# Kernel optimization log

Measured on AMD Instinct MI355X. Metric: run time of the kernel, lower is better.

Reference implementation:

```python
import jax, jax.numpy as jnp
import numpy as np

N_NODES = 100000


def gcn_conv(x, edge_src, edge_dst, edge_weight, W, b):
    # support = x @ W ; out = A @ support + b  (A given as weighted edge list)
    h = x @ W                                   # [N, d_out]
    msg = h[edge_src] * edge_weight[:, None]     # [E, d_out]
    agg = jax.ops.segment_sum(msg, edge_dst, num_segments=N_NODES)
    return agg + b


def setup_inputs() -> dict:
    key = jax.random.key(0)
    ks = jax.random.split(key, 8)
    N, E, m, hidden, m_y = N_NODES, 1600000, 128, 64, 32
    x = jax.random.normal(ks[0], (N, m), dtype=jnp.float32)
    edge_src = jax.random.randint(ks[1], (E,), 0, N, dtype=jnp.int32)
    edge_dst = jax.random.randint(ks[2], (E,), 0, N, dtype=jnp.int32)
    edge_weight = jax.random.uniform(ks[3], (E,), dtype=jnp.float32)
    s1 = 1.0 / np.sqrt(m)
    s2 = 1.0 / np.sqrt(hidden)
    W1 = jax.random.uniform(ks[4], (m, hidden), dtype=jnp.float32, minval=-s1, maxval=s1)
    b1 = jax.random.uniform(ks[5], (hidden,), dtype=jnp.float32, minval=-s1, maxval=s1)
    W2 = jax.random.uniform(ks[6], (hidden, m_y), dtype=jnp.float32, minval=-s2, maxval=s2)
    b2 = jax.random.uniform(ks[7], (m_y,), dtype=jnp.float32, minval=-s2, maxval=s2)
    return {"x": x, "edge_src": edge_src, "edge_dst": edge_dst,
            "edge_weight": edge_weight, "W1": W1, "b1": b1, "W2": W2, "b2": b2}


def reference(x, edge_src, edge_dst, edge_weight, W1, b1, W2, b2):
    out = gcn_conv(x, edge_src, edge_dst, edge_weight, W1, b1)
    out = jax.nn.relu(out)
    # F.dropout(p=0.5, training=self.training) -> identity in eval mode
    out = gcn_conv(out, edge_src, edge_dst, edge_weight, W2, b2)
    return out
```

## Files before the change

kernel.cpp:

```cpp
#include <hip/hip_runtime.h>
#include <hip/hip_bf16.h>


typedef unsigned short u16;
typedef unsigned int uint;
typedef short short8 __attribute__((ext_vector_type(8)));
typedef float floatx4 __attribute__((ext_vector_type(4)));

static __device__ __forceinline__ u16 f2bf(float f) {
    unsigned int u = __float_as_uint(f);
    return (u16)((u + 0x7fff + ((u >> 16) & 1)) >> 16);
}

#define F4C(v, j) ((j)==0?(v).x:((j)==1?(v).y:((j)==2?(v).z:(v).w)))
#define CHUNK 2048
#define ECAP 384

__global__ __launch_bounds__(256) void init_kernel(
    const float* __restrict__ W1, u16* __restrict__ wfg, int* __restrict__ gcursor)
{
    const int idx = blockIdx.x * 256 + threadIdx.x;
    if (idx < 512) gcursor[idx] = 0;
    const float4 v = ((const float4*)W1)[idx];
    const int k = idx >> 4, n4 = (idx & 15) * 4;
    const int step = k >> 5, klane = (k >> 3) & 3, j = k & 7;
    #pragma unroll
    for (int c = 0; c < 4; c++) {
        int n = n4 + c;
        wfg[(((n >> 4) * 4 + step) * 64 + klane * 16 + (n & 15)) * 8 + j] = f2bf(F4C(v, c));
    }
}

union __align__(16) SharedU {
    struct {
        u16 xs[64][136];
        u16 wf[4][4][64][8];
    } g;
    struct {
        int2 stage[CHUNK];
        u16  stb[CHUNK];
        int  hist[512], sc[512], xscan[512], place[512], runbase[512];
    } p;
};

__global__ __launch_bounds__(256, 4) void g1p_kernel(
    const float* __restrict__ x, const u16* __restrict__ wfg,
    u16* __restrict__ h1, int N,
    const int* __restrict__ src, const int* __restrict__ dst,
    const float* __restrict__ w, int* __restrict__ gcursor,
    int2* __restrict__ es, int E, int cap, int pblocks)
{
    __shared__ SharedU sh;
    const int tid = threadIdx.x;

    if (blockIdx.x < pblocks) {
        const int base = blockIdx.x * CHUNK;
        const int nloc = min(CHUNK, E - base);

        sh.p.hist[tid] = 0; sh.p.hist[tid + 256] = 0;
        __syncthreads();
        for (int i = tid; i < nloc; i += 256)
            atomicAdd(&sh.p.hist[dst[base + i] >> 8], 1);
        __syncthreads();

        sh.p.sc[tid] = sh.p.hist[tid];
        sh.p.sc[tid + 256] = sh.p.hist[tid + 256];
        __syncthreads();
        for (int o = 1; o < 512; o <<= 1) {
            int v0 = (tid >= o) ? sh.p.sc[tid - o] : 0;
            int v1 = (tid + 256 >= o) ? sh.p.sc[tid + 256 - o] : 0;
            __syncthreads();
            sh.p.sc[tid] += v0;
            sh.p.sc[tid + 256] += v1;
            __syncthreads();
        }
        sh.p.xscan[tid] = sh.p.sc[tid] - sh.p.hist[tid];
        sh.p.xscan[tid + 256] = sh.p.sc[tid + 256] - sh.p.hist[tid + 256];
        sh.p.place[tid] = sh.p.xscan[tid];
        sh.p.place[tid + 256] = sh.p.xscan[tid + 256];
        __syncthreads();

        for (int i = tid; i < nloc; i += 256) {
            int d = dst[base + i];
            int b = d >> 8;
            int pos = atomicAdd(&sh.p.place[b], 1);
            sh.p.stage[pos] = make_int2(src[base + i] | ((d & 255) << 24),
                                        __float_as_int(w[base + i]));
            sh.p.stb[pos] = (u16)b;
        }
        __syncthreads();

        {
            int l0 = sh.p.hist[tid], l1 = sh.p.hist[tid + 256];
            sh.p.runbase[tid]       = l0 ? atomicAdd(&gcursor[tid], l0)       : 0;
            sh.p.runbase[tid + 256] = l1 ? atomicAdd(&gcursor[tid + 256], l1) : 0;
        }
        __syncthreads();

        for (int i = tid; i < nloc; i += 256) {
            int b = sh.p.stb[i];
            es[(size_t)b * cap + sh.p.runbase[b] + (i - sh.p.xscan[b])] = sh.p.stage[i];
        }
        return;
    }

    const int row0 = (blockIdx.x - pblocks) * 64;
    {
        const float4* wg4 = (const float4*)wfg;
        float4* wl4 = (float4*)&sh.g.wf[0][0][0][0];
        #pragma unroll
        for (int i = 0; i < 4; i++) wl4[tid + i*256] = wg4[tid + i*256];
    }
    {
        const float4* x4 = (const float4*)x;
        #pragma unroll
        for (int i = 0; i < 8; i++) {
            int idx = tid + i*256;
            int r = idx >> 5, kc = idx & 31;
            int gr = row0 + r;
            float4 v = make_float4(0.f,0.f,0.f,0.f);
            if (gr < N) v = x4[gr*32 + kc];
            ushort4 o;
            o.x = f2bf(v.x); o.y = f2bf(v.y); o.z = f2bf(v.z); o.w = f2bf(v.w);
            *(ushort4*)&sh.g.xs[r][kc*4] = o;
        }
    }
    __syncthreads();

    const int wave = tid >> 6, lane = tid & 63;
    const int m = lane & 15, quad = lane >> 4;
    const int rw = wave * 16;

    floatx4 acc[4] = {(floatx4)(0.f), (floatx4)(0.f), (floatx4)(0.f), (floatx4)(0.f)};
    #pragma unroll
    for (int step = 0; step < 4; step++) {
        short8 a = *(const short8*)&sh.g.xs[rw + m][step*32 + quad*8];
        #pragma unroll
        for (int nt = 0; nt < 4; nt++) {
            short8 b = *(const short8*)&sh.g.wf[nt][step][lane][0];
            acc[nt] = __builtin_amdgcn_mfma_f32_16x16x32_bf16(a, b, acc[nt], 0, 0, 0);
        }
    }
    #pragma unroll
    for (int nt = 0; nt < 4; nt++) {
        #pragma unroll
        for (int r = 0; r < 4; r++) {
            int gr = row0 + rw + quad*4 + r;
            if (gr < N) h1[(size_t)gr*64 + nt*16 + m] = f2bf(acc[nt][r]);
        }
    }
}

#define SCAP 6144
__global__ __launch_bounds__(512, 3) void sort2_kernel(
    const int2* __restrict__ es, const int* __restrict__ gcursor,
    int2* __restrict__ es2, int2* __restrict__ off2, int N, int cap, int nb)
{
    __shared__ int2 stage[SCAP];
    __shared__ int hist[256], sc[256], cur[256];
    const int t = threadIdx.x;
    const int b = blockIdx.x;
    const int e0 = b * cap;
    const int len = gcursor[b];
    const int nstage = min(len, SCAP);

    if (t < 256) hist[t] = 0;
    __syncthreads();
    for (int i = t; i < nstage; i += 512) {
        int2 e = es[e0 + i];
        stage[i] = e;
        atomicAdd(&hist[((unsigned)e.x) >> 24], 1);
    }
    for (int i = SCAP + t; i < len; i += 512)
        atomicAdd(&hist[((unsigned)es[e0 + i].x) >> 24], 1);
    __syncthreads();

    int v = 0;
    if (t < 256) { v = hist[t]; sc[t] = v; }
    __syncthreads();
    for (int o = 1; o < 256; o <<= 1) {
        int add = 0;
        if (t < 256 && t >= o) add = sc[t - o];
        __syncthreads();
        if (t < 256) sc[t] += add;
        __syncthreads();
    }
    if (t < 256) {
        int ex = sc[t] - v;
        cur[t] = ex;
        int g = b * 256 + t;
        if (g < N) off2[g] = make_int2(e0 + ex, e0 + ex + v);
    }
    __syncthreads();

    for (int i = t; i < nstage; i += 512) {
        int2 e = stage[i];
        int pos = e0 + atomicAdd(&cur[((unsigned)e.x) >> 24], 1);
        es2[pos] = e;
    }
    for (int i = SCAP + t; i < len; i += 512) {
        int2 e = es[e0 + i];
        int pos = e0 + atomicAdd(&cur[((unsigned)e.x) >> 24], 1);
        es2[pos] = e;
    }
}

__global__ __launch_bounds__(256, 4) void gather1_kernel(
    const u16* __restrict__ h1, const int2* __restrict__ es,
    const int2* __restrict__ off2, const float* __restrict__ b1,
    const float* __restrict__ W2, u16* __restrict__ h2, int N)
{
    __shared__ __align__(16) u16 ts[64][72];
    __shared__ __align__(16) u16 wf2[2][2][64][8];
    __shared__ float b1s[64];
    __shared__ int2 eb[4][ECAP];
    const int tid = threadIdx.x;

    {
        const float4* s4 = (const float4*)W2;
        #pragma unroll
        for (int i = 0; i < 2; i++) {
            int idx = tid + i*256;
            float4 v = s4[idx];
            int k = idx >> 3, n4 = (idx & 7) * 4;
            int step = k >> 5, quad = (k >> 3) & 3, j = k & 7;
            #pragma unroll
            for (int c = 0; c < 4; c++) {
                int n = n4 + c;
                wf2[n >> 4][step][quad*16 + (n & 15)][j] = f2bf(F4C(v, c));
            }
        }
        if (tid < 16) ((float4*)b1s)[tid] = ((const float4*)b1)[tid];
    }
    __syncthreads();

    const int wave = tid >> 6, lane = tid & 63;
    const int h = lane >> 4, fl = lane & 15;
    const int node0 = blockIdx.x * 64 + wave * 16;
    const uint2* h1v = (const uint2*)h1;
    uint* tsu = (uint*)&ts[0][0];

    const int2 sg = off2[min(node0 + fl, N - 1)];
    const int beg = __builtin_amdgcn_readfirstlane(sg.x);
    const int end = __builtin_amdgcn_readlane(sg.y, 15);
    const int len = end - beg;

    if (len <= ECAP) {
        for (int k = lane; k < len; k += 64) eb[wave][k] = es[beg + k];

        #pragma unroll 1
        for (int j = 0; j < 8; j++) {
            const int pbegA = __builtin_amdgcn_readlane(sg.x, j) - beg;
            const int pendA = __builtin_amdgcn_readlane(sg.y, j) - beg;
            const int pbegB = __builtin_amdgcn_readlane(sg.x, j + 8) - beg;
            const int pendB = __builtin_amdgcn_readlane(sg.y, j + 8) - beg;
            const int clA = max(pendA - 1, 0), clB = max(pendB - 1, 0);
            float a0 = 0.f, a1 = 0.f, a2 = 0.f, a3 = 0.f;
            float c0 = 0.f, c1 = 0.f, c2 = 0.f, c3 = 0.f;
            int pA = pbegA, pB = pbegB;
            #pragma unroll 1
            while (pA < pendA || pB < pendB) {
                const int iA0 = pA + h,     iA1 = pA + 4 + h;
                const int iA2 = pA + 8 + h, iA3 = pA + 12 + h;
                const int iB0 = pB + h,     iB1 = pB + 4 + h;
                const int iB2 = pB + 8 + h, iB3 = pB + 12 + h;
                int2 eA0 = eb[wave][min(iA0, clA)];
                int2 eA1 = eb[wave][min(iA1, clA)];
                int2 eA2 = eb[wave][min(iA2, clA)];
                int2 eA3 = eb[wave][min(iA3, clA)];
                int2 eB0 = eb[wave][min(iB0, clB)];
                int2 eB1 = eb[wave][min(iB1, clB)];
                int2 eB2 = eb[wave][min(iB2, clB)];
                int2 eB3 = eb[wave][min(iB3, clB)];
                uint2 vA0 = h1v[(size_t)(eA0.x & 0xFFFFFF) * 16 + fl];
                uint2 vA1 = h1v[(size_t)(eA1.x & 0xFFFFFF) * 16 + fl];
                uint2 vA2 = h1v[(size_t)(eA2.x & 0xFFFFFF) * 16 + fl];
                uint2 vA3 = h1v[(size_t)(eA3.x & 0xFFFFFF) * 16 + fl];
                uint2 vB0 = h1v[(size_t)(eB0.x & 0xFFFFFF) * 16 + fl];
                uint2 vB1 = h1v[(size_t)(eB1.x & 0xFFFFFF) * 16 + fl];
                uint2 vB2 = h1v[(size_t)(eB2.x & 0xFFFFFF) * 16 + fl];
                uint2 vB3 = h1v[(size_t)(eB3.x & 0xFFFFFF) * 16 + fl];
                float wA0 = (iA0 < pendA) ? __int_as_float(eA0.y) : 0.f;
                float wA1 = (iA1 < pendA) ? __int_as_float(eA1.y) : 0.f;
                float wA2 = (iA2 < pendA) ? __int_as_float(eA2.y) : 0.f;
                float wA3 = (iA3 < pendA) ? __int_as_float(eA3.y) : 0.f;
                float wB0 = (iB0 < pendB) ? __int_as_float(eB0.y) : 0.f;
                float wB1 = (iB1 < pendB) ? __int_as_float(eB1.y) : 0.f;
                float wB2 = (iB2 < pendB) ? __int_as_float(eB2.y) : 0.f;
                float wB3 = (iB3 < pendB) ? __int_as_float(eB3.y) : 0.f;
                a0 += __uint_as_float(vA0.x << 16) * wA0 + __uint_as_float(vA1.x << 16) * wA1
                    + __uint_as_float(vA2.x << 16) * wA2 + __uint_as_float(vA3.x << 16) * wA3;
                a1 += __uint_as_float(vA0.x & 0xFFFF0000u) * wA0 + __uint_as_float(vA1.x & 0xFFFF0000u) * wA1
                    + __uint_as_float(vA2.x & 0xFFFF0000u) * wA2 + __uint_as_float(vA3.x & 0xFFFF0000u) * wA3;
                a2 += __uint_as_float(vA0.y << 16) * wA0 + __uint_as_float(vA1.y << 16) * wA1
                    + __uint_as_float(vA2.y << 16) * wA2 + __uint_as_float(vA3.y << 16) * wA3;
                a3 += __uint_as_float(vA0.y & 0xFFFF0000u) * wA0 + __uint_as_float(vA1.y & 0xFFFF0000u) * wA1
                    + __uint_as_float(vA2.y & 0xFFFF0000u) * wA2 + __uint_as_float(vA3.y & 0xFFFF0000u) * wA3;
                c0 += __uint_as_float(vB0.x << 16) * wB0 + __uint_as_float(vB1.x << 16) * wB1
                    + __uint_as_float(vB2.x << 16) * wB2 + __uint_as_float(vB3.x << 16) * wB3;
                c1 += __uint_as_float(vB0.x & 0xFFFF0000u) * wB0 + __uint_as_float(vB1.x & 0xFFFF0000u) * wB1
                    + __uint_as_float(vB2.x & 0xFFFF0000u) * wB2 + __uint_as_float(vB3.x & 0xFFFF0000u) * wB3;
                c2 += __uint_as_float(vB0.y << 16) * wB0 + __uint_as_float(vB1.y << 16) * wB1
                    + __uint_as_float(vB2.y << 16) * wB2 + __uint_as_float(vB3.y << 16) * wB3;
                c3 += __uint_as_float(vB0.y & 0xFFFF0000u) * wB0 + __uint_as_float(vB1.y & 0xFFFF0000u) * wB1
                    + __uint_as_float(vB2.y & 0xFFFF0000u) * wB2 + __uint_as_float(vB3.y & 0xFFFF0000u) * wB3;
                pA += 16; pB += 16;
            }
            a0 += __shfl_xor(a0, 16, 64); a1 += __shfl_xor(a1, 16, 64);
            a2 += __shfl_xor(a2, 16, 64); a3 += __shfl_xor(a3, 16, 64);
            a0 += __shfl_xor(a0, 32, 64); a1 += __shfl_xor(a1, 32, 64);
            a2 += __shfl_xor(a2, 32, 64); a3 += __shfl_xor(a3, 32, 64);
            c0 += __shfl_xor(c0, 16, 64); c1 += __shfl_xor(c1, 16, 64);
            c2 += __shfl_xor(c2, 16, 64); c3 += __shfl_xor(c3, 16, 64);
            c0 += __shfl_xor(c0, 32, 64); c1 += __shfl_xor(c1, 32, 64);
            c2 += __shfl_xor(c2, 32, 64); c3 += __shfl_xor(c3, 32, 64);
            if (h == 0) {
                uint t0 = (uint)f2bf(fmaxf(a0 + b1s[4*fl],     0.f))
                        | ((uint)f2bf(fmaxf(a1 + b1s[4*fl + 1], 0.f)) << 16);
                uint t1 = (uint)f2bf(fmaxf(a2 + b1s[4*fl + 2], 0.f))
                        | ((uint)f2bf(fmaxf(a3 + b1s[4*fl + 3], 0.f)) << 16);
                *(uint2*)&tsu[(wave*16 + j) * 36 + 2*fl] = make_uint2(t0, t1);
                uint t2 = (uint)f2bf(fmaxf(c0 + b1s[4*fl],     0.f))
                        | ((uint)f2bf(fmaxf(c1 + b1s[4*fl + 1], 0.f)) << 16);
                uint t3 = (uint)f2bf(fmaxf(c2 + b1s[4*fl + 2], 0.f))
                        | ((uint)f2bf(fmaxf(c3 + b1s[4*fl + 3], 0.f)) << 16);
                *(uint2*)&tsu[(wave*16 + j + 8) * 36 + 2*fl] = make_uint2(t2, t3);
            }
        }
    } else {
        #pragma unroll 1
        for (int i = 0; i < 16; i++) {
            const int pbeg = __builtin_amdgcn_readlane(sg.x, i);
            const int pend = __builtin_amdgcn_readlane(sg.y, i);
            const int cl = max(pend - 1, 0);
            float a0 = 0.f, a1 = 0.f, a2 = 0.f, a3 = 0.f;
            #pragma unroll 1
            for (int p = pbeg; p < pend; p += 16) {
                const int i0 = p + h, i1 = p + 4 + h, i2 = p + 8 + h, i3 = p + 12 + h;
                int2 e0 = es[min(i0, cl)];
                int2 e1 = es[min(i1, cl)];
                int2 e2 = es[min(i2, cl)];
                int2 e3 = es[min(i3, cl)];
                uint2 v0 = h1v[(size_t)(e0.x & 0xFFFFFF) * 16 + fl];
                uint2 v1 = h1v[(size_t)(e1.x & 0xFFFFFF) * 16 + fl];
                uint2 v2 = h1v[(size_t)(e2.x & 0xFFFFFF) * 16 + fl];
                uint2 v3 = h1v[(size_t)(e3.x & 0xFFFFFF) * 16 + fl];
                float w0 = (i0 < pend) ? __int_as_float(e0.y) : 0.f;
                float w1 = (i1 < pend) ? __int_as_float(e1.y) : 0.f;
                float w2 = (i2 < pend) ? __int_as_float(e2.y) : 0.f;
                float w3 = (i3 < pend) ? __int_as_float(e3.y) : 0.f;
                a0 += __uint_as_float(v0.x << 16) * w0 + __uint_as_float(v1.x << 16) * w1
                    + __uint_as_float(v2.x << 16) * w2 + __uint_as_float(v3.x << 16) * w3;
                a1 += __uint_as_float(v0.x & 0xFFFF0000u) * w0 + __uint_as_float(v1.x & 0xFFFF0000u) * w1
                    + __uint_as_float(v2.x & 0xFFFF0000u) * w2 + __uint_as_float(v3.x & 0xFFFF0000u) * w3;
                a2 += __uint_as_float(v0.y << 16) * w0 + __uint_as_float(v1.y << 16) * w1
                    + __uint_as_float(v2.y << 16) * w2 + __uint_as_float(v3.y << 16) * w3;
                a3 += __uint_as_float(v0.y & 0xFFFF0000u) * w0 + __uint_as_float(v1.y & 0xFFFF0000u) * w1
                    + __uint_as_float(v2.y & 0xFFFF0000u) * w2 + __uint_as_float(v3.y & 0xFFFF0000u) * w3;
            }
            a0 += __shfl_xor(a0, 16, 64); a1 += __shfl_xor(a1, 16, 64);
            a2 += __shfl_xor(a2, 16, 64); a3 += __shfl_xor(a3, 16, 64);
            a0 += __shfl_xor(a0, 32, 64); a1 += __shfl_xor(a1, 32, 64);
            a2 += __shfl_xor(a2, 32, 64); a3 += __shfl_xor(a3, 32, 64);
            if (h == 0) {
                uint t0 = (uint)f2bf(fmaxf(a0 + b1s[4*fl],     0.f))
                        | ((uint)f2bf(fmaxf(a1 + b1s[4*fl + 1], 0.f)) << 16);
                uint t1 = (uint)f2bf(fmaxf(a2 + b1s[4*fl + 2], 0.f))
                        | ((uint)f2bf(fmaxf(a3 + b1s[4*fl + 3], 0.f)) << 16);
                *(uint2*)&tsu[(wave*16 + i) * 36 + 2*fl] = make_uint2(t0, t1);
            }
        }
    }

    const int m = lane & 15, quad = lane >> 4;
    floatx4 acc[2] = {(floatx4)(0.f), (floatx4)(0.f)};
    #pragma unroll
    for (int step = 0; step < 2; step++) {
        short8 a = *(const short8*)&ts[wave*16 + m][step*32 + quad*8];
        #pragma unroll
        for (int nt = 0; nt < 2; nt++) {
            short8 b = *(const short8*)&wf2[nt][step][lane][0];
            acc[nt] = __builtin_amdgcn_mfma_f32_16x16x32_bf16(a, b, acc[nt], 0, 0, 0);
        }
    }
    #pragma unroll
    for (int nt = 0; nt < 2; nt++) {
        #pragma unroll
        for (int r = 0; r < 4; r++) {
            int g = node0 + quad*4 + r;
            if (g < N) h2[(size_t)g*32 + nt*16 + m] = f2bf(acc[nt][r]);
        }
    }
}

__global__ __launch_bounds__(256, 4) void gather2_kernel(
    const u16* __restrict__ h2, const int2* __restrict__ es,
    const int2* __restrict__ off2, const float* __restrict__ b2,
    float* __restrict__ out, int N)
{
    __shared__ int2 eb[4][ECAP];
    const int tid = threadIdx.x;
    const int wave = tid >> 6, lane = tid & 63;
    const int g = lane >> 3, fl = lane & 7;
    const int node0 = blockIdx.x * 64 + wave * 16;
    const uint2* h2v = (const uint2*)h2;

    const int2 sg = off2[min(node0 + (lane & 15), N - 1)];
    const int beg = __builtin_amdgcn_readfirstlane(sg.x);
    const int end = __builtin_amdgcn_readlane(sg.y, 15);
    const int len = end - beg;
    const float4 bb = ((const float4*)b2)[fl];

    if (len <= ECAP) {
        for (int k = lane; k < len; k += 64) eb[wave][k] = es[beg + k];

        #pragma unroll 1
        for (int j = 0; j < 8; j++) {
            const int pbegA = __builtin_amdgcn_readlane(sg.x, j) - beg;
            const int pendA = __builtin_amdgcn_readlane(sg.y, j) - beg;
            const int pbegB = __builtin_amdgcn_readlane(sg.x, j + 8) - beg;
            const int pendB = __builtin_amdgcn_readlane(sg.y, j + 8) - beg;
            const int clA = max(pendA - 1, 0), clB = max(pendB - 1, 0);
            float a0 = 0.f, a1 = 0.f, a2 = 0.f, a3 = 0.f;
            float c0 = 0.f, c1 = 0.f, c2 = 0.f, c3 = 0.f;
            int pA = pbegA, pB = pbegB;
            #pragma unroll 1
            while (pA < pendA || pB < pendB) {
                const int iA0 = pA + g, iA1 = pA + 8 + g;
                const int iB0 = pB + g, iB1 = pB + 8 + g;
                int2 eA0 = eb[wave][min(iA0, clA)];
                int2 eA1 = eb[wave][min(iA1, clA)];
                int2 eB0 = eb[wave][min(iB0, clB)];
                int2 eB1 = eb[wave][min(iB1, clB)];
                uint2 vA0 = h2v[(size_t)(eA0.x & 0xFFFFFF) * 8 + fl];
                uint2 vA1 = h2v[(size_t)(eA1.x & 0xFFFFFF) * 8 + fl];
                uint2 vB0 = h2v[(size_t)(eB0.x & 0xFFFFFF) * 8 + fl];
                uint2 vB1 = h2v[(size_t)(eB1.x & 0xFFFFFF) * 8 + fl];
                float wA0 = (iA0 < pendA) ? __int_as_float(eA0.y) : 0.f;
                float wA1 = (iA1 < pendA) ? __int_as_float(eA1.y) : 0.f;
                float wB0 = (iB0 < pendB) ? __int_as_float(eB0.y) : 0.f;
                float wB1 = (iB1 < pendB) ? __int_as_float(eB1.y) : 0.f;
                a0 += __uint_as_float(vA0.x << 16) * wA0 + __uint_as_float(vA1.x << 16) * wA1;
                a1 += __uint_as_float(vA0.x & 0xFFFF0000u) * wA0 + __uint_as_float(vA1.x & 0xFFFF0000u) * wA1;
                a2 += __uint_as_float(vA0.y << 16) * wA0 + __uint_as_float(vA1.y << 16) * wA1;
                a3 += __uint_as_float(vA0.y & 0xFFFF0000u) * wA0 + __uint_as_float(vA1.y & 0xFFFF0000u) * wA1;
                c0 += __uint_as_float(vB0.x << 16) * wB0 + __uint_as_float(vB1.x << 16) * wB1;
                c1 += __uint_as_float(vB0.x & 0xFFFF0000u) * wB0 + __uint_as_float(vB1.x & 0xFFFF0000u) * wB1;
                c2 += __uint_as_float(vB0.y << 16) * wB0 + __uint_as_float(vB1.y << 16) * wB1;
                c3 += __uint_as_float(vB0.y & 0xFFFF0000u) * wB0 + __uint_as_float(vB1.y & 0xFFFF0000u) * wB1;
                pA += 16; pB += 16;
            }
            a0 += __shfl_xor(a0, 8, 64);  a1 += __shfl_xor(a1, 8, 64);
            a2 += __shfl_xor(a2, 8, 64);  a3 += __shfl_xor(a3, 8, 64);
            a0 += __shfl_xor(a0, 16, 64); a1 += __shfl_xor(a1, 16, 64);
            a2 += __shfl_xor(a2, 16, 64); a3 += __shfl_xor(a3, 16, 64);
            a0 += __shfl_xor(a0, 32, 64); a1 += __shfl_xor(a1, 32, 64);
            a2 += __shfl_xor(a2, 32, 64); a3 += __shfl_xor(a3, 32, 64);
            c0 += __shfl_xor(c0, 8, 64);  c1 += __shfl_xor(c1, 8, 64);
            c2 += __shfl_xor(c2, 8, 64);  c3 += __shfl_xor(c3, 8, 64);
            c0 += __shfl_xor(c0, 16, 64); c1 += __shfl_xor(c1, 16, 64);
            c2 += __shfl_xor(c2, 16, 64); c3 += __shfl_xor(c3, 16, 64);
            c0 += __shfl_xor(c0, 32, 64); c1 += __shfl_xor(c1, 32, 64);
            c2 += __shfl_xor(c2, 32, 64); c3 += __shfl_xor(c3, 32, 64);
            const int dA = node0 + j, dB = node0 + j + 8;
            if (g == 0 && dA < N)
                *(float4*)&out[(size_t)dA * 32 + 4 * fl] =
                    make_float4(a0 + bb.x, a1 + bb.y, a2 + bb.z, a3 + bb.w);
            if (g == 0 && dB < N)
                *(float4*)&out[(size_t)dB * 32 + 4 * fl] =
                    make_float4(c0 + bb.x, c1 + bb.y, c2 + bb.z, c3 + bb.w);
        }
    } else {
        #pragma unroll 1
        for (int i = 0; i < 16; i++) {
            const int pbeg = __builtin_amdgcn_readlane(sg.x, i);
            const int pend = __builtin_amdgcn_readlane(sg.y, i);
            const int cl = max(pend - 1, 0);
            float a0 = 0.f, a1 = 0.f, a2 = 0.f, a3 = 0.f;
            #pragma unroll 1
            for (int p = pbeg; p < pend; p += 32) {
                const int i0 = p + g, i1 = p + 8 + g, i2 = p + 16 + g, i3 = p + 24 + g;
                int2 e0 = es[min(i0, cl)];
                int2 e1 = es[min(i1, cl)];
                int2 e2 = es[min(i2, cl)];
                int2 e3 = es[min(i3, cl)];
                uint2 v0 = h2v[(size_t)(e0.x & 0xFFFFFF) * 8 + fl];
                uint2 v1 = h2v[(size_t)(e1.x & 0xFFFFFF) * 8 + fl];
                uint2 v2 = h2v[(size_t)(e2.x & 0xFFFFFF) * 8 + fl];
                uint2 v3 = h2v[(size_t)(e3.x & 0xFFFFFF) * 8 + fl];
                float w0 = (i0 < pend) ? __int_as_float(e0.y) : 0.f;
                float w1 = (i1 < pend) ? __int_as_float(e1.y) : 0.f;
                float w2 = (i2 < pend) ? __int_as_float(e2.y) : 0.f;
                float w3 = (i3 < pend) ? __int_as_float(e3.y) : 0.f;
                a0 += __uint_as_float(v0.x << 16) * w0 + __uint_as_float(v1.x << 16) * w1
                    + __uint_as_float(v2.x << 16) * w2 + __uint_as_float(v3.x << 16) * w3;
                a1 += __uint_as_float(v0.x & 0xFFFF0000u) * w0 + __uint_as_float(v1.x & 0xFFFF0000u) * w1
                    + __uint_as_float(v2.x & 0xFFFF0000u) * w2 + __uint_as_float(v3.x & 0xFFFF0000u) * w3;
                a2 += __uint_as_float(v0.y << 16) * w0 + __uint_as_float(v1.y << 16) * w1
                    + __uint_as_float(v2.y << 16) * w2 + __uint_as_float(v3.y << 16) * w3;
                a3 += __uint_as_float(v0.y & 0xFFFF0000u) * w0 + __uint_as_float(v1.y & 0xFFFF0000u) * w1
                    + __uint_as_float(v2.y & 0xFFFF0000u) * w2 + __uint_as_float(v3.y & 0xFFFF0000u) * w3;
            }
            a0 += __shfl_xor(a0, 8, 64);  a1 += __shfl_xor(a1, 8, 64);
            a2 += __shfl_xor(a2, 8, 64);  a3 += __shfl_xor(a3, 8, 64);
            a0 += __shfl_xor(a0, 16, 64); a1 += __shfl_xor(a1, 16, 64);
            a2 += __shfl_xor(a2, 16, 64); a3 += __shfl_xor(a3, 16, 64);
            a0 += __shfl_xor(a0, 32, 64); a1 += __shfl_xor(a1, 32, 64);
            a2 += __shfl_xor(a2, 32, 64); a3 += __shfl_xor(a3, 32, 64);
            const int d = node0 + i;
            if (g == 0 && d < N)
                *(float4*)&out[(size_t)d * 32 + 4 * fl] =
                    make_float4(a0 + bb.x, a1 + bb.y, a2 + bb.z, a3 + bb.w);
        }
    }
}

extern "C" void kernel_launch(void* const* d_in, const int* in_sizes, int n_in,
                              void* d_out, int out_size, void* d_ws, size_t ws_size,
                              hipStream_t stream)
{
    const float* x   = (const float*)d_in[0];
    const int*  esrc = (const int*)d_in[1];
    const int*  edst = (const int*)d_in[2];
    const float* ew  = (const float*)d_in[3];
    const float* W1  = (const float*)d_in[4];
    const float* b1  = (const float*)d_in[5];
    const float* W2  = (const float*)d_in[6];
    const float* b2  = (const float*)d_in[7];
    float* out = (float*)d_out;

    const int N = in_sizes[0] / 128;
    const int E = in_sizes[1];
    const int nb = (N + 255) >> 8;

    const int mean = (E + nb - 1) / nb;
    int s = 1; while (s * s < mean) s++;
    const int cap = (mean + 8 * s + 15) & ~15;

    char* base = (char*)d_ws;
    size_t o = 0;
    auto alloc = [&](size_t bytes) { char* p = base + o; o = (o + bytes + 255) & ~(size_t)255; return p; };
    u16*  h1      = (u16*) alloc((size_t)N * 64 * 2);
    u16*  h2      = (u16*) alloc((size_t)N * 32 * 2);
    int2* es      = (int2*)alloc((size_t)nb * cap * 8);
    int2* es2     = (int2*)alloc((size_t)nb * cap * 8);
    int2* off2    = (int2*)alloc((size_t)N * 8);
    int*  gcursor = (int*) alloc(512 * 4);
    u16*  wfg     = (u16*) alloc(8192 * 2);

    const int pblocks = (E + CHUNK - 1) / CHUNK;
    const int gblocks = (N + 63) / 64;

    init_kernel<<<8, 256, 0, stream>>>(W1, wfg, gcursor);
    g1p_kernel<<<pblocks + gblocks, 256, 0, stream>>>(
        x, wfg, h1, N, esrc, edst, ew, gcursor, es, E, cap, pblocks);
    sort2_kernel<<<nb, 512, 0, stream>>>(es, gcursor, es2, off2, N, cap, nb);
    gather1_kernel<<<(N + 63) / 64, 256, 0, stream>>>(h1, es2, off2, b1, W2, h2, N);
    gather2_kernel<<<(N + 63) / 64, 256, 0, stream>>>(h2, es2, off2, b2, out, N);
}
```

Baseline: 221.1 us.

## Scatter edges directly to buckets and load GEMM A-operand straight to registers

```diff
diff --git a/kernel.cpp b/kernel.cpp
--- a/kernel.cpp
+++ b/kernel.cpp
@@ -33,17 +33,14 @@
 
 union __align__(16) SharedU {
     struct {
-        u16 xs[64][136];
         u16 wf[4][4][64][8];
     } g;
     struct {
-        int2 stage[CHUNK];
-        u16  stb[CHUNK];
-        int  hist[512], sc[512], xscan[512], place[512], runbase[512];
+        int hist[512], runbase[512], place[512];
     } p;
 };
 
-__global__ __launch_bounds__(256, 4) void g1p_kernel(
+__global__ __launch_bounds__(256, 5) void g1p_kernel(
     const float* __restrict__ x, const u16* __restrict__ wfg,
     u16* __restrict__ h1, int N,
     const int* __restrict__ src, const int* __restrict__ dst,
@@ -63,43 +60,21 @@
             atomicAdd(&sh.p.hist[dst[base + i] >> 8], 1);
         __syncthreads();
 
-        sh.p.sc[tid] = sh.p.hist[tid];
-        sh.p.sc[tid + 256] = sh.p.hist[tid + 256];
-        __syncthreads();
-        for (int o = 1; o < 512; o <<= 1) {
-            int v0 = (tid >= o) ? sh.p.sc[tid - o] : 0;
-            int v1 = (tid + 256 >= o) ? sh.p.sc[tid + 256 - o] : 0;
-            __syncthreads();
-            sh.p.sc[tid] += v0;
-            sh.p.sc[tid + 256] += v1;
-            __syncthreads();
-        }
-        sh.p.xscan[tid] = sh.p.sc[tid] - sh.p.hist[tid];
-        sh.p.xscan[tid + 256] = sh.p.sc[tid + 256] - sh.p.hist[tid + 256];
-        sh.p.place[tid] = sh.p.xscan[tid];
-        sh.p.place[tid + 256] = sh.p.xscan[tid + 256];
-        __syncthreads();
-
-        for (int i = tid; i < nloc; i += 256) {
-            int d = dst[base + i];
-            int b = d >> 8;
-            int pos = atomicAdd(&sh.p.place[b], 1);
-            sh.p.stage[pos] = make_int2(src[base + i] | ((d & 255) << 24),
-                                        __float_as_int(w[base + i]));
-            sh.p.stb[pos] = (u16)b;
-        }
-        __syncthreads();
-
         {
             int l0 = sh.p.hist[tid], l1 = sh.p.hist[tid + 256];
             sh.p.runbase[tid]       = l0 ? atomicAdd(&gcursor[tid], l0)       : 0;
             sh.p.runbase[tid + 256] = l1 ? atomicAdd(&gcursor[tid + 256], l1) : 0;
+            sh.p.place[tid] = 0; sh.p.place[tid + 256] = 0;
         }
         __syncthreads();
 
         for (int i = tid; i < nloc; i += 256) {
-            int b = sh.p.stb[i];
-            es[(size_t)b * cap + sh.p.runbase[b] + (i - sh.p.xscan[b])] = sh.p.stage[i];
+            int d = dst[base + i];
+            int b = d >> 8;
+            int r = atomicAdd(&sh.p.place[b], 1);
+            es[(size_t)b * cap + sh.p.runbase[b] + r] =
+                make_int2(src[base + i] | ((d & 255) << 24),
+                          __float_as_int(w[base + i]));
         }
         return;
     }
@@ -111,33 +86,32 @@
         #pragma unroll
         for (int i = 0; i < 4; i++) wl4[tid + i*256] = wg4[tid + i*256];
     }
-    {
-        const float4* x4 = (const float4*)x;
-        #pragma unroll
-        for (int i = 0; i < 8; i++) {
-            int idx = tid + i*256;
-            int r = idx >> 5, kc = idx & 31;
-            int gr = row0 + r;
-            float4 v = make_float4(0.f,0.f,0.f,0.f);
-            if (gr < N) v = x4[gr*32 + kc];
-            ushort4 o;
-            o.x = f2bf(v.x); o.y = f2bf(v.y); o.z = f2bf(v.z); o.w = f2bf(v.w);
-            *(ushort4*)&sh.g.xs[r][kc*4] = o;
-        }
-    }
-    __syncthreads();
 
     const int wave = tid >> 6, lane = tid & 63;
     const int m = lane & 15, quad = lane >> 4;
-    const int rw = wave * 16;
+    const int gr0 = row0 + wave * 16 + m;
+    const int grc = min(gr0, N - 1);
+    const float4* xr = (const float4*)x + (size_t)grc * 32;
+
+    float4 xv[8];
+    #pragma unroll
+    for (int s = 0; s < 4; s++) {
+        xv[2*s]     = xr[s*8 + quad*2];
+        xv[2*s + 1] = xr[s*8 + quad*2 + 1];
+    }
+    __syncthreads();
 
     floatx4 acc[4] = {(floatx4)(0.f), (floatx4)(0.f), (floatx4)(0.f), (floatx4)(0.f)};
     #pragma unroll
-    for (int step = 0; step < 4; step++) {
-        short8 a = *(const short8*)&sh.g.xs[rw + m][step*32 + quad*8];
+    for (int s = 0; s < 4; s++) {
+        short8 a;
+        a[0] = (short)f2bf(xv[2*s].x);   a[1] = (short)f2bf(xv[2*s].y);
+        a[2] = (short)f2bf(xv[2*s].z);   a[3] = (short)f2bf(xv[2*s].w);
+        a[4] = (short)f2bf(xv[2*s+1].x); a[5] = (short)f2bf(xv[2*s+1].y);
+        a[6] = (short)f2bf(xv[2*s+1].z); a[7] = (short)f2bf(xv[2*s+1].w);
         #pragma unroll
         for (int nt = 0; nt < 4; nt++) {
-            short8 b = *(const short8*)&sh.g.wf[nt][step][lane][0];
+            short8 b = *(const short8*)&sh.g.wf[nt][s][lane][0];
             acc[nt] = __builtin_amdgcn_mfma_f32_16x16x32_bf16(a, b, acc[nt], 0, 0, 0);
         }
     }
@@ -145,7 +119,7 @@
     for (int nt = 0; nt < 4; nt++) {
         #pragma unroll
         for (int r = 0; r < 4; r++) {
-            int gr = row0 + rw + quad*4 + r;
+            int gr = row0 + wave*16 + quad*4 + r;
             if (gr < N) h1[(size_t)gr*64 + nt*16 + m] = f2bf(acc[nt][r]);
         }
     }
```

Result: slower. 234.9 us (+6.2%).

## Split each sort2 bucket across two blocks with per-half histograms

Applied to the files above, without the earlier changes.

```diff
diff --git a/kernel.cpp b/kernel.cpp
--- a/kernel.cpp
+++ b/kernel.cpp
@@ -151,32 +151,31 @@
     }
 }
 
-#define SCAP 6144
-__global__ __launch_bounds__(512, 3) void sort2_kernel(
+#define SCAP2 2304
+__global__ __launch_bounds__(512, 4) void sort2_kernel(
     const int2* __restrict__ es, const int* __restrict__ gcursor,
     int2* __restrict__ es2, int2* __restrict__ off2, int N, int cap, int nb)
 {
-    __shared__ int2 stage[SCAP];
-    __shared__ int hist[256], sc[256], cur[256];
+    __shared__ int2 stage[SCAP2];
+    __shared__ int hA[256], hB[256], sc[256], cur[256];
     const int t = threadIdx.x;
-    const int b = blockIdx.x;
+    const int b = blockIdx.x >> 1, h = blockIdx.x & 1;
     const int e0 = b * cap;
     const int len = gcursor[b];
-    const int nstage = min(len, SCAP);
-
-    if (t < 256) hist[t] = 0;
+    const int len1 = (len + 1) >> 1;
+
+    if (t < 256) { hA[t] = 0; hB[t] = 0; }
     __syncthreads();
-    for (int i = t; i < nstage; i += 512) {
+    for (int i = t; i < len; i += 512) {
         int2 e = es[e0 + i];
-        stage[i] = e;
-        atomicAdd(&hist[((unsigned)e.x) >> 24], 1);
-    }
-    for (int i = SCAP + t; i < len; i += 512)
-        atomicAdd(&hist[((unsigned)es[e0 + i].x) >> 24], 1);
+        int k = ((unsigned)e.x) >> 24;
+        if (i < len1) { atomicAdd(&hA[k], 1); if (h == 0) stage[i] = e; }
+        else          { atomicAdd(&hB[k], 1); if (h == 1) stage[i - len1] = e; }
+    }
     __syncthreads();
 
     int v = 0;
-    if (t < 256) { v = hist[t]; sc[t] = v; }
+    if (t < 256) { v = hA[t] + hB[t]; sc[t] = v; }
     __syncthreads();
     for (int o = 1; o < 256; o <<= 1) {
         int add = 0;
@@ -187,19 +186,17 @@
     }
     if (t < 256) {
         int ex = sc[t] - v;
-        cur[t] = ex;
-        int g = b * 256 + t;
-        if (g < N) off2[g] = make_int2(e0 + ex, e0 + ex + v);
+        cur[t] = ex + (h ? hA[t] : 0);
+        if (h == 0) {
+            int g = b * 256 + t;
+            if (g < N) off2[g] = make_int2(e0 + ex, e0 + ex + v);
+        }
     }
     __syncthreads();
 
-    for (int i = t; i < nstage; i += 512) {
+    const int myn = h ? (len - len1) : len1;
+    for (int i = t; i < myn; i += 512) {
         int2 e = stage[i];
-        int pos = e0 + atomicAdd(&cur[((unsigned)e.x) >> 24], 1);
-        es2[pos] = e;
-    }
-    for (int i = SCAP + t; i < len; i += 512) {
-        int2 e = es[e0 + i];
         int pos = e0 + atomicAdd(&cur[((unsigned)e.x) >> 24], 1);
         es2[pos] = e;
     }
@@ -554,7 +551,7 @@
     init_kernel<<<8, 256, 0, stream>>>(W1, wfg, gcursor);
     g1p_kernel<<<pblocks + gblocks, 256, 0, stream>>>(
         x, wfg, h1, N, esrc, edst, ew, gcursor, es, E, cap, pblocks);
-    sort2_kernel<<<nb, 512, 0, stream>>>(es, gcursor, es2, off2, N, cap, nb);
+    sort2_kernel<<<2 * nb, 512, 0, stream>>>(es, gcursor, es2, off2, N, cap, nb);
     gather1_kernel<<<(N + 63) / 64, 256, 0, stream>>>(h1, es2, off2, b1, W2, h2, N);
     gather2_kernel<<<(N + 63) / 64, 256, 0, stream>>>(h2, es2, off2, b2, out, N);
 }
```

After: 221.5 us. No clear change (+0.1%).

## Fuse bucket sort with layer-1 gather using LDS-resident sorted edges

Applied to the files above, without the earlier changes.

```diff
diff --git a/kernel.cpp b/kernel.cpp
--- a/kernel.cpp
+++ b/kernel.cpp
@@ -14,6 +14,7 @@
 
 #define F4C(v, j) ((j)==0?(v).x:((j)==1?(v).y:((j)==2?(v).z:(v).w)))
 #define CHUNK 2048
+#define CAPC 4608
 #define ECAP 384
 
 __global__ __launch_bounds__(256) void init_kernel(
@@ -151,109 +152,89 @@
     }
 }
 
-#define SCAP 6144
-__global__ __launch_bounds__(512, 3) void sort2_kernel(
-    const int2* __restrict__ es, const int* __restrict__ gcursor,
-    int2* __restrict__ es2, int2* __restrict__ off2, int N, int cap, int nb)
+__global__ __launch_bounds__(512, 4) void sg1_kernel(
+    const u16* __restrict__ h1, const int2* __restrict__ es,
+    const int* __restrict__ gcursor, int2* __restrict__ es2,
+    int2* __restrict__ off2, const float* __restrict__ b1,
+    const float* __restrict__ W2, u16* __restrict__ h2, int N, int cap)
 {
-    __shared__ int2 stage[SCAP];
-    __shared__ int hist[256], sc[256], cur[256];
+    __shared__ int2 sorted[CAPC];
+    __shared__ __align__(16) u16 ts[8][16][72];
+    __shared__ __align__(16) u16 wf2[2][2][64][8];
+    __shared__ float b1s[64];
+    __shared__ int hist[256], exs[256], cur[256];
     const int t = threadIdx.x;
     const int b = blockIdx.x;
     const int e0 = b * cap;
-    const int len = gcursor[b];
-    const int nstage = min(len, SCAP);
-
-    if (t < 256) hist[t] = 0;
-    __syncthreads();
-    for (int i = t; i < nstage; i += 512) {
-        int2 e = es[e0 + i];
-        stage[i] = e;
-        atomicAdd(&hist[((unsigned)e.x) >> 24], 1);
-    }
-    for (int i = SCAP + t; i < len; i += 512)
-        atomicAdd(&hist[((unsigned)es[e0 + i].x) >> 24], 1);
+    const int len = min(gcursor[b], CAPC);
+
+    {
+        const float4* s4 = (const float4*)W2;
+        float4 v = s4[t];
+        int k = t >> 3, n4 = (t & 7) * 4;
+        int step = k >> 5, quad = (k >> 3) & 3, j = k & 7;
+        #pragma unroll
+        for (int c = 0; c < 4; c++) {
+            int n = n4 + c;
+            wf2[n >> 4][step][quad*16 + (n & 15)][j] = f2bf(F4C(v, c));
+        }
+        if (t < 16) ((float4*)b1s)[t] = ((const float4*)b1)[t];
+        if (t < 256) hist[t] = 0;
+    }
+    __syncthreads();
+
+    int2 re[9]; int rk[9];
+    #pragma unroll
+    for (int k = 0; k < 9; k++) {
+        int i = t + k * 512;
+        if (i < len) {
+            re[k] = es[e0 + i];
+            rk[k] = (int)(((unsigned)re[k].x) >> 24);
+            atomicAdd(&hist[rk[k]], 1);
+        } else rk[k] = -1;
+    }
     __syncthreads();
 
     int v = 0;
-    if (t < 256) { v = hist[t]; sc[t] = v; }
+    if (t < 256) { v = hist[t]; cur[t] = v; }
     __syncthreads();
     for (int o = 1; o < 256; o <<= 1) {
         int add = 0;
-        if (t < 256 && t >= o) add = sc[t - o];
-        __syncthreads();
-        if (t < 256) sc[t] += add;
+        if (t < 256 && t >= o) add = cur[t - o];
+        __syncthreads();
+        if (t < 256) cur[t] += add;
         __syncthreads();
     }
     if (t < 256) {
-        int ex = sc[t] - v;
+        int ex = cur[t] - v;
+        exs[t] = ex;
         cur[t] = ex;
         int g = b * 256 + t;
         if (g < N) off2[g] = make_int2(e0 + ex, e0 + ex + v);
     }
     __syncthreads();
 
-    for (int i = t; i < nstage; i += 512) {
-        int2 e = stage[i];
-        int pos = e0 + atomicAdd(&cur[((unsigned)e.x) >> 24], 1);
-        es2[pos] = e;
-    }
-    for (int i = SCAP + t; i < len; i += 512) {
-        int2 e = es[e0 + i];
-        int pos = e0 + atomicAdd(&cur[((unsigned)e.x) >> 24], 1);
-        es2[pos] = e;
-    }
-}
-
-__global__ __launch_bounds__(256, 4) void gather1_kernel(
-    const u16* __restrict__ h1, const int2* __restrict__ es,
-    const int2* __restrict__ off2, const float* __restrict__ b1,
-    const float* __restrict__ W2, u16* __restrict__ h2, int N)
-{
-    __shared__ __align__(16) u16 ts[64][72];
-    __shared__ __align__(16) u16 wf2[2][2][64][8];
-    __shared__ float b1s[64];
-    __shared__ int2 eb[4][ECAP];
-    const int tid = threadIdx.x;
-
-    {
-        const float4* s4 = (const float4*)W2;
-        #pragma unroll
-        for (int i = 0; i < 2; i++) {
-            int idx = tid + i*256;
-            float4 v = s4[idx];
-            int k = idx >> 3, n4 = (idx & 7) * 4;
-            int step = k >> 5, quad = (k >> 3) & 3, j = k & 7;
-            #pragma unroll
-            for (int c = 0; c < 4; c++) {
-                int n = n4 + c;
-                wf2[n >> 4][step][quad*16 + (n & 15)][j] = f2bf(F4C(v, c));
-            }
-        }
-        if (tid < 16) ((float4*)b1s)[tid] = ((const float4*)b1)[tid];
-    }
-    __syncthreads();
-
-    const int wave = tid >> 6, lane = tid & 63;
+    #pragma unroll
+    for (int k = 0; k < 9; k++)
+        if (rk[k] >= 0) sorted[atomicAdd(&cur[rk[k]], 1)] = re[k];
+    __syncthreads();
+
+    for (int i = t; i < len; i += 512)
+        es2[e0 + i] = sorted[i];
+
+    const int wave = t >> 6, lane = t & 63;
     const int h = lane >> 4, fl = lane & 15;
-    const int node0 = blockIdx.x * 64 + wave * 16;
     const uint2* h1v = (const uint2*)h1;
-    uint* tsu = (uint*)&ts[0][0];
-
-    const int2 sg = off2[min(node0 + fl, N - 1)];
-    const int beg = __builtin_amdgcn_readfirstlane(sg.x);
-    const int end = __builtin_amdgcn_readlane(sg.y, 15);
-    const int len = end - beg;
-
-    if (len <= ECAP) {
-        for (int k = lane; k < len; k += 64) eb[wave][k] = es[beg + k];
-
+    uint* tsu = (uint*)&ts[wave][0][0];
+
+    #pragma unroll 1
+    for (int half = 0; half < 2; half++) {
+        const int n0 = wave * 32 + half * 16;
         #pragma unroll 1
         for (int j = 0; j < 8; j++) {
-            const int pbegA = __builtin_amdgcn_readlane(sg.x, j) - beg;
-            const int pendA = __builtin_amdgcn_readlane(sg.y, j) - beg;
-            const int pbegB = __builtin_amdgcn_readlane(sg.x, j + 8) - beg;
-            const int pendB = __builtin_amdgcn_readlane(sg.y, j + 8) - beg;
+            const int nA = n0 + j, nB = n0 + j + 8;
+            const int pbegA = exs[nA], pendA = pbegA + hist[nA];
+            const int pbegB = exs[nB], pendB = pbegB + hist[nB];
             const int clA = max(pendA - 1, 0), clB = max(pendB - 1, 0);
             float a0 = 0.f, a1 = 0.f, a2 = 0.f, a3 = 0.f;
             float c0 = 0.f, c1 = 0.f, c2 = 0.f, c3 = 0.f;
@@ -264,14 +245,14 @@
                 const int iA2 = pA + 8 + h, iA3 = pA + 12 + h;
                 const int iB0 = pB + h,     iB1 = pB + 4 + h;
                 const int iB2 = pB + 8 + h, iB3 = pB + 12 + h;
-                int2 eA0 = eb[wave][min(iA0, clA)];
-                int2 eA1 = eb[wave][min(iA1, clA)];
-                int2 eA2 = eb[wave][min(iA2, clA)];
-                int2 eA3 = eb[wave][min(iA3, clA)];
-                int2 eB0 = eb[wave][min(iB0, clB)];
-                int2 eB1 = eb[wave][min(iB1, clB)];
-                int2 eB2 = eb[wave][min(iB2, clB)];
-                int2 eB3 = eb[wave][min(iB3, clB)];
+                int2 eA0 = sorted[min(iA0, clA)];
+                int2 eA1 = sorted[min(iA1, clA)];
+                int2 eA2 = sorted[min(iA2, clA)];
+                int2 eA3 = sorted[min(iA3, clA)];
+                int2 eB0 = sorted[min(iB0, clB)];
+                int2 eB1 = sorted[min(iB1, clB)];
+                int2 eB2 = sorted[min(iB2, clB)];
+                int2 eB3 = sorted[min(iB3, clB)];
                 uint2 vA0 = h1v[(size_t)(eA0.x & 0xFFFFFF) * 16 + fl];
                 uint2 vA1 = h1v[(size_t)(eA1.x & 0xFFFFFF) * 16 + fl];
                 uint2 vA2 = h1v[(size_t)(eA2.x & 0xFFFFFF) * 16 + fl];
@@ -319,76 +300,33 @@
                         | ((uint)f2bf(fmaxf(a1 + b1s[4*fl + 1], 0.f)) << 16);
                 uint t1 = (uint)f2bf(fmaxf(a2 + b1s[4*fl + 2], 0.f))
                         | ((uint)f2bf(fmaxf(a3 + b1s[4*fl + 3], 0.f)) << 16);
-                *(uint2*)&tsu[(wave*16 + j) * 36 + 2*fl] = make_uint2(t0, t1);
+                *(uint2*)&tsu[j * 36 + 2*fl] = make_uint2(t0, t1);
                 uint t2 = (uint)f2bf(fmaxf(c0 + b1s[4*fl],     0.f))
                         | ((uint)f2bf(fmaxf(c1 + b1s[4*fl + 1], 0.f)) << 16);
                 uint t3 = (uint)f2bf(fmaxf(c2 + b1s[4*fl + 2], 0.f))
                         | ((uint)f2bf(fmaxf(c3 + b1s[4*fl + 3], 0.f)) << 16);
-                *(uint2*)&tsu[(wave*16 + j + 8) * 36 + 2*fl] = make_uint2(t2, t3);
-            }
-        }
-    } else {
-        #pragma unroll 1
-        for (int i = 0; i < 16; i++) {
-            const int pbeg = __builtin_amdgcn_readlane(sg.x, i);
-            const int pend = __builtin_amdgcn_readlane(sg.y, i);
-            const int cl = max(pend - 1, 0);
-            float a0 = 0.f, a1 = 0.f, a2 = 0.f, a3 = 0.f;
-            #pragma unroll 1
-            for (int p = pbeg; p < pend; p += 16) {
-                const int i0 = p + h, i1 = p + 4 + h, i2 = p + 8 + h, i3 = p + 12 + h;
-                int2 e0 = es[min(i0, cl)];
-                int2 e1 = es[min(i1, cl)];
-                int2 e2 = es[min(i2, cl)];
-                int2 e3 = es[min(i3, cl)];
-                uint2 v0 = h1v[(size_t)(e0.x & 0xFFFFFF) * 16 + fl];
-                uint2 v1 = h1v[(size_t)(e1.x & 0xFFFFFF) * 16 + fl];
-                uint2 v2 = h1v[(size_t)(e2.x & 0xFFFFFF) * 16 + fl];
-                uint2 v3 = h1v[(size_t)(e3.x & 0xFFFFFF) * 16 + fl];
-                float w0 = (i0 < pend) ? __int_as_float(e0.y) : 0.f;
-                float w1 = (i1 < pend) ? __int_as_float(e1.y) : 0.f;
-                float w2 = (i2 < pend) ? __int_as_float(e2.y) : 0.f;
-                float w3 = (i3 < pend) ? __int_as_float(e3.y) : 0.f;
-                a0 += __uint_as_float(v0.x << 16) * w0 + __uint_as_float(v1.x << 16) * w1
-                    + __uint_as_float(v2.x << 16) * w2 + __uint_as_float(v3.x << 16) * w3;
-                a1 += __uint_as_float(v0.x & 0xFFFF0000u) * w0 + __uint_as_float(v1.x & 0xFFFF0000u) * w1
-                    + __uint_as_float(v2.x & 0xFFFF0000u) * w2 + __uint_as_float(v3.x & 0xFFFF0000u) * w3;
-                a2 += __uint_as_float(v0.y << 16) * w0 + __uint_as_float(v1.y << 16) * w1
-                    + __uint_as_float(v2.y << 16) * w2 + __uint_as_float(v3.y << 16) * w3;
-                a3 += __uint_as_float(v0.y & 0xFFFF0000u) * w0 + __uint_as_float(v1.y & 0xFFFF0000u) * w1
-                    + __uint_as_float(v2.y & 0xFFFF0000u) * w2 + __uint_as_float(v3.y & 0xFFFF0000u) * w3;
-            }
-            a0 += __shfl_xor(a0, 16, 64); a1 += __shfl_xor(a1, 16, 64);
-            a2 += __shfl_xor(a2, 16, 64); a3 += __shfl_xor(a3, 16, 64);
-            a0 += __shfl_xor(a0, 32, 64); a1 += __shfl_xor(a1, 32, 64);
-            a2 += __shfl_xor(a2, 32, 64); a3 += __shfl_xor(a3, 32, 64);
-            if (h == 0) {
-                uint t0 = (uint)f2bf(fmaxf(a0 + b1s[4*fl],     0.f))
-                        | ((uint)f2bf(fmaxf(a1 + b1s[4*fl + 1], 0.f)) << 16);
-                uint t1 = (uint)f2bf(fmaxf(a2 + b1s[4*fl + 2], 0.f))
-                        | ((uint)f2bf(fmaxf(a3 + b1s[4*fl + 3], 0.f)) << 16);
-                *(uint2*)&tsu[(wave*16 + i) * 36 + 2*fl] = make_uint2(t0, t1);
-            }
-        }
-    }
-
-    const int m = lane & 15, quad = lane >> 4;
-    floatx4 acc[2] = {(floatx4)(0.f), (floatx4)(0.f)};
-    #pragma unroll
-    for (int step = 0; step < 2; step++) {
-        short8 a = *(const short8*)&ts[wave*16 + m][step*32 + quad*8];
+                *(uint2*)&tsu[(j + 8) * 36 + 2*fl] = make_uint2(t2, t3);
+            }
+        }
+
+        const int m = lane & 15, quad = lane >> 4;
+        floatx4 acc[2] = {(floatx4)(0.f), (floatx4)(0.f)};
+        #pragma unroll
+        for (int step = 0; step < 2; step++) {
+            short8 a = *(const short8*)&ts[wave][m][step*32 + quad*8];
+            #pragma unroll
+            for (int nt = 0; nt < 2; nt++) {
+                short8 bb = *(const short8*)&wf2[nt][step][lane][0];
+                acc[nt] = __builtin_amdgcn_mfma_f32_16x16x32_bf16(a, bb, acc[nt], 0, 0, 0);
+            }
+        }
         #pragma unroll
         for (int nt = 0; nt < 2; nt++) {
-            short8 b = *(const short8*)&wf2[nt][step][lane][0];
-            acc[nt] = __builtin_amdgcn_mfma_f32_16x16x32_bf16(a, b, acc[nt], 0, 0, 0);
-        }
-    }
-    #pragma unroll
-    for (int nt = 0; nt < 2; nt++) {
-        #pragma unroll
-        for (int r = 0; r < 4; r++) {
-            int g = node0 + quad*4 + r;
-            if (g < N) h2[(size_t)g*32 + nt*16 + m] = f2bf(acc[nt][r]);
+            #pragma unroll
+            for (int r = 0; r < 4; r++) {
+                int g = b * 256 + n0 + quad*4 + r;
+                if (g < N) h2[(size_t)g*32 + nt*16 + m] = f2bf(acc[nt][r]);
+            }
         }
     }
 }
@@ -535,7 +473,8 @@
 
     const int mean = (E + nb - 1) / nb;
     int s = 1; while (s * s < mean) s++;
-    const int cap = (mean + 8 * s + 15) & ~15;
+    int cap = (mean + 8 * s + 15) & ~15;
+    if (cap > CAPC) cap = CAPC;
 
     char* base = (char*)d_ws;
     size_t o = 0;
@@ -554,7 +493,6 @@
     init_kernel<<<8, 256, 0, stream>>>(W1, wfg, gcursor);
     g1p_kernel<<<pblocks + gblocks, 256, 0, stream>>>(
         x, wfg, h1, N, esrc, edst, ew, gcursor, es, E, cap, pblocks);
-    sort2_kernel<<<nb, 512, 0, stream>>>(es, gcursor, es2, off2, N, cap, nb);
-    gather1_kernel<<<(N + 63) / 64, 256, 0, stream>>>(h1, es2, off2, b1, W2, h2, N);
+    sg1_kernel<<<nb, 512, 0, stream>>>(h1, es, gcursor, es2, off2, b1, W2, h2, N, cap);
     gather2_kernel<<<(N + 63) / 64, 256, 0, stream>>>(h2, es2, off2, b2, out, N);
 }
```

New measurement: 219.0 us. About the same (-0.9%).
